# Performance work log

Measured on AMD Instinct MI355X. Metric: run time of the kernel, lower is better.

The kernel has to match this reference:

```python
import jax, jax.numpy as jnp
import numpy as np
from jax.ops import segment_sum

N_NODES = 50000
N_EDGES = 800000
IN_DIM, HID_DIM, OUT_DIM = 128, 256, 128


def _glorot(key, shape):
    lim = np.sqrt(6.0 / (shape[0] + shape[1]))
    return jax.random.uniform(key, shape, jnp.float32, -lim, lim)


def setup_inputs() -> dict:
    key = jax.random.key(0)
    ks = jax.random.split(key, 4)
    x = jax.random.normal(ks[0], (N_NODES, IN_DIM), jnp.float32)
    edge_index = jax.random.randint(ks[1], (2, N_EDGES), 0, N_NODES, jnp.int64)
    W1 = _glorot(ks[2], (IN_DIM, HID_DIM))
    b1 = jnp.zeros((HID_DIM,), jnp.float32)
    W2 = _glorot(ks[3], (HID_DIM, OUT_DIM))
    b2 = jnp.zeros((OUT_DIM,), jnp.float32)
    return {"x": x, "edge_index": edge_index, "W1": W1, "b1": b1, "W2": W2, "b2": b2}


def gcn_conv(x, W, b, src, dst, n_nodes):
    # PyG GCNConv: x' = D^{-1/2} (A + I) D^{-1/2} (x W) + b
    h = x @ W  # [N, F_out]
    deg = segment_sum(jnp.ones_like(src, dtype=h.dtype), dst, num_segments=n_nodes) + 1.0  # +1 self loop
    dinv = jax.lax.rsqrt(deg)  # [N]
    norm = dinv[src] * dinv[dst]  # per-edge norm [E]
    msg = h[src] * norm[:, None]  # [E, F_out]
    agg = segment_sum(msg, dst, num_segments=n_nodes)
    agg = agg + h * (dinv * dinv)[:, None]  # self-loop term: norm_ii = dinv_i^2
    return agg + b


def reference(x, edge_index, W1, b1, W2, b2):
    src, dst = edge_index[0], edge_index[1]
    h = gcn_conv(x, W1, b1, src, dst, N_NODES)
    h = jax.nn.relu(h)
    out = gcn_conv(h, W2, b2, src, dst, N_NODES)
    return out
```

## Files before the change

kernel.cpp:

```cpp
#include <hip/hip_runtime.h>

#define N_NODES 50000
#define N_EDGES 800000
#define IN_DIM  128
#define HID_DIM 256
#define OUT_DIM 128
#define BUCKET_CAP 64
#define NCOARSE 391
#define BINSZ 128
#define CHUNK 4000
#define NBLK1 200
#define SEGCAP 32
#define HLD 264
#define GROWS 64

typedef __attribute__((ext_vector_type(8))) short short8;
typedef __attribute__((ext_vector_type(4))) float f32x4;

__device__ inline ushort f2b(float f) {
    union { float f; unsigned u; } v; v.f = f;
    return (ushort)((v.u + 0x7FFFu + ((v.u >> 16) & 1u)) >> 16);
}
__device__ inline float b2f(ushort h) {
    union { unsigned u; float f; } v; v.u = ((unsigned)h) << 16;
    return v.f;
}
__device__ inline float2 u2f2(unsigned u) {
    float2 r; r.x = b2f((ushort)(u & 0xFFFFu)); r.y = b2f((ushort)(u >> 16)); return r;
}
__device__ inline unsigned f2u2(float a, float b) {
    return (unsigned)f2b(a) | ((unsigned)f2b(b) << 16);
}
__device__ inline void fma8(float2* acc, uint4 u, float n) {
    float2 v0 = u2f2(u.x), v1 = u2f2(u.y), v2 = u2f2(u.z), v3 = u2f2(u.w);
    acc[0].x += v0.x * n; acc[0].y += v0.y * n;
    acc[1].x += v1.x * n; acc[1].y += v1.y * n;
    acc[2].x += v2.x * n; acc[2].y += v2.y * n;
    acc[3].x += v3.x * n; acc[3].y += v3.y * n;
}


__global__ __launch_bounds__(256) void prep_kernel(const float* __restrict__ x,
                                                   const float* __restrict__ W1,
                                                   const float* __restrict__ W2,
                                                   const int* __restrict__ src,
                                                   const int* __restrict__ dst,
                                                   ushort* __restrict__ xb,
                                                   ushort* __restrict__ w1t,
                                                   ushort* __restrict__ w2t,
                                                   int* __restrict__ bcnt,
                                                   int* __restrict__ binbuf) {
    __shared__ int vals[CHUNK];
    __shared__ ushort lpos[CHUNK];
    __shared__ ushort lbin[CHUNK];
    __shared__ int hist[NCOARSE];
    const int b = blockIdx.x;
    const int t = threadIdx.x;
    if (b < 6250) {
        int i = b * 256 + t;
        float4 v = ((const float4*)x)[i];
        ushort4 o; o.x = f2b(v.x); o.y = f2b(v.y); o.z = f2b(v.z); o.w = f2b(v.w);
        ((ushort4*)xb)[i] = o;
    } else if (b < 6506) {
        int i = (b - 6250) * 256 + t;
        if (i < 32768) {
            int n = i >> 7, k = i & 127;
            w1t[i] = f2b(W1[k * HID_DIM + n]);
        } else {
            int j = i - 32768;
            int n = j >> 8, k = j & 255;
            w2t[j] = f2b(W2[k * OUT_DIM + n]);
        }
    } else {
        const int blk = b - 6506;
        const int e0 = blk * CHUNK;
        for (int i = t; i < NCOARSE; i += 256) hist[i] = 0;
        __syncthreads();
        for (int i = t; i < CHUNK; i += 256) {
            int s = src[e0 + i], d = dst[e0 + i];
            int bin = d >> 7;
            vals[i] = (s << 7) | (d & 127);
            lbin[i] = (ushort)bin;
            lpos[i] = (ushort)atomicAdd(&hist[bin], 1);
        }
        __syncthreads();
        for (int i = t; i < NCOARSE; i += 256) {
            int h = hist[i]; if (h > SEGCAP) h = SEGCAP;
            bcnt[i * NBLK1 + blk] = h;
        }
        for (int i = t; i < CHUNK; i += 256) {
            int bin = lbin[i];
            int p = lpos[i];
            if (p < SEGCAP) binbuf[((size_t)bin * NBLK1 + blk) * SEGCAP + p] = vals[i];
        }
    }
}


__global__ __launch_bounds__(256) void binpass2_kernel(const int* __restrict__ bcnt,
                                                       const int* __restrict__ binbuf,
                                                       int* __restrict__ cnt,
                                                       float* __restrict__ dinv,
                                                       int* __restrict__ bucket) {
    __shared__ int lcnt[BINSZ];
    __shared__ int lm[NBLK1];
    __shared__ int lbuck[BINSZ * BUCKET_CAP];
    const int bin = blockIdx.x;
    const int t = threadIdx.x;
    if (t < BINSZ) lcnt[t] = 0;
    if (t < NBLK1) lm[t] = bcnt[bin * NBLK1 + t];
    __syncthreads();
    const int* bb = binbuf + (size_t)bin * NBLK1 * SEGCAP;
    for (int f = t; f < NBLK1 * SEGCAP; f += 256) {
        int blk = f >> 5;
        int sl = f & 31;
        if (sl < lm[blk]) {
            int v = bb[f];
            int dl = v & 127;
            int pos = atomicAdd(&lcnt[dl], 1);
            if (pos < BUCKET_CAP) lbuck[dl * BUCKET_CAP + pos] = v >> 7;
        }
    }
    __syncthreads();
    const int node0 = bin * BINSZ;
    int node = node0 + t;
    if (t < BINSZ && node < N_NODES) {
        int c = lcnt[t] > BUCKET_CAP ? BUCKET_CAP : lcnt[t];
        cnt[node] = c;
        dinv[node] = rsqrtf((float)c + 1.0f);
    }
    int nvalid = N_NODES - node0; if (nvalid > BINSZ) nvalid = BINSZ;
    if (nvalid <= 0) return;
    int total4 = (nvalid * BUCKET_CAP) >> 2;
    int4* d4 = (int4*)(bucket + (size_t)node0 * BUCKET_CAP);
    const int4* s4 = (const int4*)lbuck;
    for (int j = t; j < total4; j += 256) d4[j] = s4[j];
}


__global__ __launch_bounds__(256) void gather0_kernel(const int* __restrict__ cnt,
                                                      const int* __restrict__ bucket,
                                                      const float* __restrict__ dinv,
                                                      const ushort* __restrict__ xb,
                                                      ushort* __restrict__ aggxb) {
    const int w = blockIdx.x * 4 + (threadIdx.x >> 6);
    const int lane = threadIdx.x & 63;
    const int grp = lane >> 4, sub = lane & 15;
    const int n = cnt[w];
    const float dd = dinv[w];
    int sv = 0; float nv = 0.f;
    if (lane < n) { sv = bucket[w * BUCKET_CAP + lane]; nv = dinv[sv] * dd; }

    float2 acc[4];
    if (grp == 0) {
        uint4 su = ((const uint4*)(xb + (size_t)w * IN_DIM))[sub];
        float sd = dd * dd;
        acc[0] = u2f2(su.x); acc[1] = u2f2(su.y); acc[2] = u2f2(su.z); acc[3] = u2f2(su.w);
#pragma unroll
        for (int j = 0; j < 4; ++j) { acc[j].x *= sd; acc[j].y *= sd; }
    } else {
#pragma unroll
        for (int j = 0; j < 4; ++j) acc[j] = {0.f, 0.f};
    }

    const int nr = (n + 15) & ~15;
    for (int i = 0; i < nr; i += 16) {
        int s0 = __shfl(sv, i + grp),      s1 = __shfl(sv, i + 4 + grp);
        int s2 = __shfl(sv, i + 8 + grp),  s3 = __shfl(sv, i + 12 + grp);
        float n0 = __shfl(nv, i + grp),     n1 = __shfl(nv, i + 4 + grp);
        float n2 = __shfl(nv, i + 8 + grp), n3 = __shfl(nv, i + 12 + grp);
        uint4 u0 = ((const uint4*)(xb + (size_t)s0 * IN_DIM))[sub];
        uint4 u1 = ((const uint4*)(xb + (size_t)s1 * IN_DIM))[sub];
        uint4 u2 = ((const uint4*)(xb + (size_t)s2 * IN_DIM))[sub];
        uint4 u3 = ((const uint4*)(xb + (size_t)s3 * IN_DIM))[sub];
        fma8(acc, u0, n0); fma8(acc, u1, n1); fma8(acc, u2, n2); fma8(acc, u3, n3);
    }
#pragma unroll
    for (int j = 0; j < 4; ++j) {
        acc[j].x += __shfl_down(acc[j].x, 32); acc[j].y += __shfl_down(acc[j].y, 32);
        acc[j].x += __shfl_down(acc[j].x, 16); acc[j].y += __shfl_down(acc[j].y, 16);
    }
    if (lane < 16) {
        uint4 o = {f2u2(acc[0].x, acc[0].y), f2u2(acc[1].x, acc[1].y),
                   f2u2(acc[2].x, acc[2].y), f2u2(acc[3].x, acc[3].y)};
        ((uint4*)(aggxb + (size_t)w * IN_DIM))[sub] = o;
    }
}


__global__ __launch_bounds__(256, 2) void gemm12_mfma(const ushort* __restrict__ aggxb,
                                                      const ushort* __restrict__ w1t,
                                                      const float* __restrict__ b1,
                                                      const ushort* __restrict__ w2t,
                                                      ushort* __restrict__ h2b) {
    __shared__ ushort Hs[GROWS * HLD];
    const int row0 = blockIdx.x * GROWS;
    const int wv = threadIdx.x >> 6;
    const int lane = threadIdx.x & 63;
    const int l15 = lane & 15, q = lane >> 4;

    short8 bf1[16];
#pragma unroll
    for (int kb = 0; kb < 4; ++kb)
#pragma unroll
        for (int t = 0; t < 4; ++t) {
            int col = wv * 64 + t * 16 + l15;
            bf1[kb * 4 + t] = *(const short8*)(w1t + (size_t)col * IN_DIM + kb * 32 + q * 8);
        }
    short8 af[4][4];
#pragma unroll
    for (int sub = 0; sub < 4; ++sub) {
        int ar = row0 + sub * 16 + l15;
        if (ar >= N_NODES) ar = N_NODES - 1;
        const ushort* ab = aggxb + (size_t)ar * IN_DIM + q * 8;
#pragma unroll
        for (int kb = 0; kb < 4; ++kb) af[sub][kb] = *(const short8*)(ab + kb * 32);
    }
    f32x4 acc1[4][4] = {};
#pragma unroll
    for (int sub = 0; sub < 4; ++sub)
#pragma unroll
        for (int kb = 0; kb < 4; ++kb)
#pragma unroll
            for (int t = 0; t < 4; ++t)
                acc1[sub][t] = __builtin_amdgcn_mfma_f32_16x16x32_bf16(
                    af[sub][kb], bf1[kb * 4 + t], acc1[sub][t], 0, 0, 0);
#pragma unroll
    for (int t = 0; t < 4; ++t) {
        int col = wv * 64 + t * 16 + l15;
        float bias = b1[col];
#pragma unroll
        for (int sub = 0; sub < 4; ++sub)
#pragma unroll
            for (int r = 0; r < 4; ++r) {
                int row = sub * 16 + q * 4 + r;
                float v = acc1[sub][t][r] + bias;
                Hs[row * HLD + col] = f2b(v > 0.f ? v : 0.f);
            }
    }
    __syncthreads();

    short8 bf2[16];
#pragma unroll
    for (int kb = 0; kb < 8; ++kb)
#pragma unroll
        for (int t = 0; t < 2; ++t) {
            int col = wv * 32 + t * 16 + l15;
            bf2[kb * 2 + t] = *(const short8*)(w2t + (size_t)col * HID_DIM + kb * 32 + q * 8);
        }
    f32x4 acc2[4][2] = {};
#pragma unroll
    for (int sub = 0; sub < 4; ++sub) {
        const ushort* hb = Hs + (sub * 16 + l15) * HLD + q * 8;
#pragma unroll
        for (int kb = 0; kb < 8; ++kb) {
            short8 a = *(const short8*)(hb + kb * 32);
#pragma unroll
            for (int t = 0; t < 2; ++t)
                acc2[sub][t] = __builtin_amdgcn_mfma_f32_16x16x32_bf16(
                    a, bf2[kb * 2 + t], acc2[sub][t], 0, 0, 0);
        }
    }
#pragma unroll
    for (int sub = 0; sub < 4; ++sub)
#pragma unroll
        for (int t = 0; t < 2; ++t) {
            int col = wv * 32 + t * 16 + l15;
#pragma unroll
            for (int r = 0; r < 4; ++r) {
                int row = row0 + sub * 16 + q * 4 + r;
                if (row < N_NODES)
                    h2b[(size_t)row * OUT_DIM + col] = f2b(acc2[sub][t][r]);
            }
        }
}


__global__ __launch_bounds__(256) void gather2_kernel(const int* __restrict__ cnt,
                                                      const int* __restrict__ bucket,
                                                      const float* __restrict__ dinv,
                                                      const ushort* __restrict__ h2b,
                                                      const float* __restrict__ b2,
                                                      float* __restrict__ out) {
    const int w = blockIdx.x * 4 + (threadIdx.x >> 6);
    const int lane = threadIdx.x & 63;
    const int grp = lane >> 4, sub = lane & 15;
    const int n = cnt[w];
    const float dd = dinv[w];
    int sv = 0; float nv = 0.f;
    if (lane < n) { sv = bucket[w * BUCKET_CAP + lane]; nv = dinv[sv] * dd; }

    float2 acc[4];
    if (grp == 0) {
        uint4 su = ((const uint4*)(h2b + (size_t)w * OUT_DIM))[sub];
        float sd = dd * dd;
        acc[0] = u2f2(su.x); acc[1] = u2f2(su.y); acc[2] = u2f2(su.z); acc[3] = u2f2(su.w);
#pragma unroll
        for (int j = 0; j < 4; ++j) { acc[j].x *= sd; acc[j].y *= sd; }
    } else {
#pragma unroll
        for (int j = 0; j < 4; ++j) acc[j] = {0.f, 0.f};
    }

    const int nr = (n + 15) & ~15;
    for (int i = 0; i < nr; i += 16) {
        int s0 = __shfl(sv, i + grp),      s1 = __shfl(sv, i + 4 + grp);
        int s2 = __shfl(sv, i + 8 + grp),  s3 = __shfl(sv, i + 12 + grp);
        float n0 = __shfl(nv, i + grp),     n1 = __shfl(nv, i + 4 + grp);
        float n2 = __shfl(nv, i + 8 + grp), n3 = __shfl(nv, i + 12 + grp);
        uint4 u0 = ((const uint4*)(h2b + (size_t)s0 * OUT_DIM))[sub];
        uint4 u1 = ((const uint4*)(h2b + (size_t)s1 * OUT_DIM))[sub];
        uint4 u2 = ((const uint4*)(h2b + (size_t)s2 * OUT_DIM))[sub];
        uint4 u3 = ((const uint4*)(h2b + (size_t)s3 * OUT_DIM))[sub];
        fma8(acc, u0, n0); fma8(acc, u1, n1); fma8(acc, u2, n2); fma8(acc, u3, n3);
    }
#pragma unroll
    for (int j = 0; j < 4; ++j) {
        acc[j].x += __shfl_down(acc[j].x, 32); acc[j].y += __shfl_down(acc[j].y, 32);
        acc[j].x += __shfl_down(acc[j].x, 16); acc[j].y += __shfl_down(acc[j].y, 16);
    }
    if (lane < 16) {
        const float4* bp = (const float4*)b2;
        float4 b0 = bp[sub * 2], b1v = bp[sub * 2 + 1];
        float4 o0 = {acc[0].x + b0.x, acc[0].y + b0.y, acc[1].x + b0.z, acc[1].y + b0.w};
        float4 o1 = {acc[2].x + b1v.x, acc[2].y + b1v.y, acc[3].x + b1v.z, acc[3].y + b1v.w};
        float4* op = (float4*)(out + (size_t)w * OUT_DIM);
        op[sub * 2] = o0;
        op[sub * 2 + 1] = o1;
    }
}

extern "C" void kernel_launch(void* const* d_in, const int* in_sizes, int n_in,
                              void* d_out, int out_size, void* d_ws, size_t ws_size,
                              hipStream_t stream) {
    const float* x  = (const float*)d_in[0];
    const int*   ei = (const int*)d_in[1];
    const float* W1 = (const float*)d_in[2];
    const float* b1 = (const float*)d_in[3];
    const float* W2 = (const float*)d_in[4];
    const float* b2 = (const float*)d_in[5];
    float* out = (float*)d_out;

    const int* src = ei;
    const int* dst = ei + N_EDGES;

    char* ws = (char*)d_ws;
    int*    bcnt   = (int*)(ws);
    int*    cnt    = (int*)(ws + 320000);
    float*  dinv   = (float*)(ws + 520000);
    int*    bucket = (int*)(ws + 720000);
    int*    binbuf = (int*)(ws + 13520000);
    ushort* xb     = (ushort*)(ws + 23532800);
    ushort* w1t    = (ushort*)(ws + 36332800);
    ushort* w2t    = (ushort*)(ws + 36398336);
    ushort* aggxb  = (ushort*)(ws + 36463872);
    ushort* h2b    = (ushort*)(ws + 49263872);

    prep_kernel<<<6706, 256, 0, stream>>>(x, W1, W2, src, dst, xb, w1t, w2t, bcnt, binbuf);
    binpass2_kernel<<<NCOARSE, 256, 0, stream>>>(bcnt, binbuf, cnt, dinv, bucket);

    gather0_kernel<<<N_NODES / 4, 256, 0, stream>>>(cnt, bucket, dinv, xb, aggxb);
    gemm12_mfma<<<(N_NODES + GROWS - 1) / GROWS, 256, 0, stream>>>(aggxb, w1t, b1, w2t, h2b);

    gather2_kernel<<<N_NODES / 4, 256, 0, stream>>>(cnt, bucket, dinv, h2b, b2, out);
}
```

Before: 206.4 us.

## Fuse first-layer neighbor gather into the dual GEMM kernel via shared memory

The separate gather0 kernel is removed. Its aggregation of x rows is now done inside the GEMM kernel, with each wave gathering 16 rows into an LDS tile that then feeds the MFMA layer-1 product. This drops the global write and re-read of the aggregated feature buffer and one kernel launch. In exchange, gather parallelism falls to 782 blocks with serialized per-row loops per wave, and the extra LDS may reduce occupancy, so latency hiding for the random gathers may suffer.

```diff
diff --git a/kernel.cpp b/kernel.cpp
--- a/kernel.cpp
+++ b/kernel.cpp
@@ -12,6 +12,7 @@
 #define NBLK1 200
 #define SEGCAP 32
 #define HLD 264
+#define AXLD 136
 #define GROWS 64
 
 typedef __attribute__((ext_vector_type(8))) short short8;
@@ -38,6 +39,7 @@
     acc[2].x += v2.x * n; acc[2].y += v2.y * n;
     acc[3].x += v3.x * n; acc[3].y += v3.y * n;
 }
+
 
 
 __global__ __launch_bounds__(256) void prep_kernel(const float* __restrict__ x,
@@ -138,66 +140,67 @@
 }
 
 
-__global__ __launch_bounds__(256) void gather0_kernel(const int* __restrict__ cnt,
-                                                      const int* __restrict__ bucket,
-                                                      const float* __restrict__ dinv,
-                                                      const ushort* __restrict__ xb,
-                                                      ushort* __restrict__ aggxb) {
-    const int w = blockIdx.x * 4 + (threadIdx.x >> 6);
-    const int lane = threadIdx.x & 63;
-    const int grp = lane >> 4, sub = lane & 15;
-    const int n = cnt[w];
-    const float dd = dinv[w];
-    int sv = 0; float nv = 0.f;
-    if (lane < n) { sv = bucket[w * BUCKET_CAP + lane]; nv = dinv[sv] * dd; }
-
-    float2 acc[4];
-    if (grp == 0) {
-        uint4 su = ((const uint4*)(xb + (size_t)w * IN_DIM))[sub];
-        float sd = dd * dd;
-        acc[0] = u2f2(su.x); acc[1] = u2f2(su.y); acc[2] = u2f2(su.z); acc[3] = u2f2(su.w);
-#pragma unroll
-        for (int j = 0; j < 4; ++j) { acc[j].x *= sd; acc[j].y *= sd; }
-    } else {
-#pragma unroll
-        for (int j = 0; j < 4; ++j) acc[j] = {0.f, 0.f};
-    }
-
-    const int nr = (n + 15) & ~15;
-    for (int i = 0; i < nr; i += 16) {
-        int s0 = __shfl(sv, i + grp),      s1 = __shfl(sv, i + 4 + grp);
-        int s2 = __shfl(sv, i + 8 + grp),  s3 = __shfl(sv, i + 12 + grp);
-        float n0 = __shfl(nv, i + grp),     n1 = __shfl(nv, i + 4 + grp);
-        float n2 = __shfl(nv, i + 8 + grp), n3 = __shfl(nv, i + 12 + grp);
-        uint4 u0 = ((const uint4*)(xb + (size_t)s0 * IN_DIM))[sub];
-        uint4 u1 = ((const uint4*)(xb + (size_t)s1 * IN_DIM))[sub];
-        uint4 u2 = ((const uint4*)(xb + (size_t)s2 * IN_DIM))[sub];
-        uint4 u3 = ((const uint4*)(xb + (size_t)s3 * IN_DIM))[sub];
-        fma8(acc, u0, n0); fma8(acc, u1, n1); fma8(acc, u2, n2); fma8(acc, u3, n3);
-    }
-#pragma unroll
-    for (int j = 0; j < 4; ++j) {
-        acc[j].x += __shfl_down(acc[j].x, 32); acc[j].y += __shfl_down(acc[j].y, 32);
-        acc[j].x += __shfl_down(acc[j].x, 16); acc[j].y += __shfl_down(acc[j].y, 16);
-    }
-    if (lane < 16) {
-        uint4 o = {f2u2(acc[0].x, acc[0].y), f2u2(acc[1].x, acc[1].y),
-                   f2u2(acc[2].x, acc[2].y), f2u2(acc[3].x, acc[3].y)};
-        ((uint4*)(aggxb + (size_t)w * IN_DIM))[sub] = o;
-    }
-}
-
-
-__global__ __launch_bounds__(256, 2) void gemm12_mfma(const ushort* __restrict__ aggxb,
-                                                      const ushort* __restrict__ w1t,
-                                                      const float* __restrict__ b1,
-                                                      const ushort* __restrict__ w2t,
-                                                      ushort* __restrict__ h2b) {
+__global__ __launch_bounds__(256, 2) void gemm12_fused(const int* __restrict__ cnt,
+                                                       const int* __restrict__ bucket,
+                                                       const float* __restrict__ dinv,
+                                                       const ushort* __restrict__ xb,
+                                                       const ushort* __restrict__ w1t,
+                                                       const float* __restrict__ b1,
+                                                       const ushort* __restrict__ w2t,
+                                                       ushort* __restrict__ h2b) {
+    __shared__ ushort Axs[GROWS * AXLD];
     __shared__ ushort Hs[GROWS * HLD];
     const int row0 = blockIdx.x * GROWS;
     const int wv = threadIdx.x >> 6;
     const int lane = threadIdx.x & 63;
+    const int grp = lane >> 4, sub = lane & 15;
     const int l15 = lane & 15, q = lane >> 4;
+
+    for (int j = 0; j < 16; ++j) {
+        int w = row0 + wv * 16 + j;
+        bool valid = w < N_NODES;
+        int wc = valid ? w : 0;
+        int n = valid ? cnt[wc] : 0;
+        float dd = valid ? dinv[wc] : 0.f;
+        int sv = 0; float nv = 0.f;
+        if (lane < n) { sv = bucket[wc * BUCKET_CAP + lane]; nv = dinv[sv] * dd; }
+
+        float2 acc[4];
+        if (grp == 0) {
+            uint4 su = ((const uint4*)(xb + (size_t)wc * IN_DIM))[sub];
+            float sd = dd * dd;
+            acc[0] = u2f2(su.x); acc[1] = u2f2(su.y); acc[2] = u2f2(su.z); acc[3] = u2f2(su.w);
+#pragma unroll
+            for (int k = 0; k < 4; ++k) { acc[k].x *= sd; acc[k].y *= sd; }
+        } else {
+#pragma unroll
+            for (int k = 0; k < 4; ++k) acc[k] = {0.f, 0.f};
+        }
+
+        const int nr = (n + 15) & ~15;
+        for (int i = 0; i < nr; i += 16) {
+            int s0 = __shfl(sv, i + grp),      s1 = __shfl(sv, i + 4 + grp);
+            int s2 = __shfl(sv, i + 8 + grp),  s3 = __shfl(sv, i + 12 + grp);
+            float n0 = __shfl(nv, i + grp),     n1 = __shfl(nv, i + 4 + grp);
+            float n2 = __shfl(nv, i + 8 + grp), n3 = __shfl(nv, i + 12 + grp);
+            uint4 u0 = ((const uint4*)(xb + (size_t)s0 * IN_DIM))[sub];
+            uint4 u1 = ((const uint4*)(xb + (size_t)s1 * IN_DIM))[sub];
+            uint4 u2 = ((const uint4*)(xb + (size_t)s2 * IN_DIM))[sub];
+            uint4 u3 = ((const uint4*)(xb + (size_t)s3 * IN_DIM))[sub];
+            fma8(acc, u0, n0); fma8(acc, u1, n1); fma8(acc, u2, n2); fma8(acc, u3, n3);
+        }
+#pragma unroll
+        for (int k = 0; k < 4; ++k) {
+            acc[k].x += __shfl_down(acc[k].x, 32); acc[k].y += __shfl_down(acc[k].y, 32);
+            acc[k].x += __shfl_down(acc[k].x, 16); acc[k].y += __shfl_down(acc[k].y, 16);
+        }
+        if (lane < 16) {
+            uint4 o = {f2u2(acc[0].x, acc[0].y), f2u2(acc[1].x, acc[1].y),
+                       f2u2(acc[2].x, acc[2].y), f2u2(acc[3].x, acc[3].y)};
+            ((uint4*)(Axs + (wv * 16 + j) * AXLD))[sub] = o;
+        }
+    }
+    __syncthreads();
 
     short8 bf1[16];
 #pragma unroll
@@ -209,32 +212,30 @@
         }
     short8 af[4][4];
 #pragma unroll
-    for (int sub = 0; sub < 4; ++sub) {
-        int ar = row0 + sub * 16 + l15;
-        if (ar >= N_NODES) ar = N_NODES - 1;
-        const ushort* ab = aggxb + (size_t)ar * IN_DIM + q * 8;
-#pragma unroll
-        for (int kb = 0; kb < 4; ++kb) af[sub][kb] = *(const short8*)(ab + kb * 32);
+    for (int sub2 = 0; sub2 < 4; ++sub2) {
+        const ushort* ab = Axs + (sub2 * 16 + l15) * AXLD + q * 8;
+#pragma unroll
+        for (int kb = 0; kb < 4; ++kb) af[sub2][kb] = *(const short8*)(ab + kb * 32);
     }
     f32x4 acc1[4][4] = {};
 #pragma unroll
-    for (int sub = 0; sub < 4; ++sub)
+    for (int sub2 = 0; sub2 < 4; ++sub2)
 #pragma unroll
         for (int kb = 0; kb < 4; ++kb)
 #pragma unroll
             for (int t = 0; t < 4; ++t)
-                acc1[sub][t] = __builtin_amdgcn_mfma_f32_16x16x32_bf16(
-                    af[sub][kb], bf1[kb * 4 + t], acc1[sub][t], 0, 0, 0);
+                acc1[sub2][t] = __builtin_amdgcn_mfma_f32_16x16x32_bf16(
+                    af[sub2][kb], bf1[kb * 4 + t], acc1[sub2][t], 0, 0, 0);
 #pragma unroll
     for (int t = 0; t < 4; ++t) {
         int col = wv * 64 + t * 16 + l15;
         float bias = b1[col];
 #pragma unroll
-        for (int sub = 0; sub < 4; ++sub)
+        for (int sub2 = 0; sub2 < 4; ++sub2)
 #pragma unroll
             for (int r = 0; r < 4; ++r) {
-                int row = sub * 16 + q * 4 + r;
-                float v = acc1[sub][t][r] + bias;
+                int row = sub2 * 16 + q * 4 + r;
+                float v = acc1[sub2][t][r] + bias;
                 Hs[row * HLD + col] = f2b(v > 0.f ? v : 0.f);
             }
     }
@@ -250,27 +251,27 @@
         }
     f32x4 acc2[4][2] = {};
 #pragma unroll
-    for (int sub = 0; sub < 4; ++sub) {
-        const ushort* hb = Hs + (sub * 16 + l15) * HLD + q * 8;
+    for (int sub2 = 0; sub2 < 4; ++sub2) {
+        const ushort* hb = Hs + (sub2 * 16 + l15) * HLD + q * 8;
 #pragma unroll
         for (int kb = 0; kb < 8; ++kb) {
             short8 a = *(const short8*)(hb + kb * 32);
 #pragma unroll
             for (int t = 0; t < 2; ++t)
-                acc2[sub][t] = __builtin_amdgcn_mfma_f32_16x16x32_bf16(
-                    a, bf2[kb * 2 + t], acc2[sub][t], 0, 0, 0);
-        }
-    }
-#pragma unroll
-    for (int sub = 0; sub < 4; ++sub)
+                acc2[sub2][t] = __builtin_amdgcn_mfma_f32_16x16x32_bf16(
+                    a, bf2[kb * 2 + t], acc2[sub2][t], 0, 0, 0);
+        }
+    }
+#pragma unroll
+    for (int sub2 = 0; sub2 < 4; ++sub2)
 #pragma unroll
         for (int t = 0; t < 2; ++t) {
             int col = wv * 32 + t * 16 + l15;
 #pragma unroll
             for (int r = 0; r < 4; ++r) {
-                int row = row0 + sub * 16 + q * 4 + r;
+                int row = row0 + sub2 * 16 + q * 4 + r;
                 if (row < N_NODES)
-                    h2b[(size_t)row * OUT_DIM + col] = f2b(acc2[sub][t][r]);
+                    h2b[(size_t)row * OUT_DIM + col] = f2b(acc2[sub2][t][r]);
             }
         }
 }
@@ -353,14 +354,13 @@
     ushort* xb     = (ushort*)(ws + 23532800);
     ushort* w1t    = (ushort*)(ws + 36332800);
     ushort* w2t    = (ushort*)(ws + 36398336);
-    ushort* aggxb  = (ushort*)(ws + 36463872);
-    ushort* h2b    = (ushort*)(ws + 49263872);
+    ushort* h2b    = (ushort*)(ws + 36463872);
 
     prep_kernel<<<6706, 256, 0, stream>>>(x, W1, W2, src, dst, xb, w1t, w2t, bcnt, binbuf);
     binpass2_kernel<<<NCOARSE, 256, 0, stream>>>(bcnt, binbuf, cnt, dinv, bucket);
 
-    gather0_kernel<<<N_NODES / 4, 256, 0, stream>>>(cnt, bucket, dinv, xb, aggxb);
-    gemm12_mfma<<<(N_NODES + GROWS - 1) / GROWS, 256, 0, stream>>>(aggxb, w1t, b1, w2t, h2b);
+    gemm12_fused<<<(N_NODES + GROWS - 1) / GROWS, 256, 0, stream>>>(
+        cnt, bucket, dinv, xb, w1t, b1, w2t, h2b);
 
     gather2_kernel<<<N_NODES / 4, 256, 0, stream>>>(cnt, bucket, dinv, h2b, b2, out);
 }
```

Result: slower. 235.8 us (+14.3%).
